# Kernel optimization log

Measured on AMD Instinct MI355X. Metric: run time of the kernel, lower is better.

Reference implementation:

```python
import jax, jax.numpy as jnp
import numpy as np

B = 2
SP = (480, 360, 32)   # spatial_shape (z, y, x)
GS = (8, 8, 8)        # query_gs_ratio
EP = (40, 15, 16)     # embed_params (pool compress ratio)
H = 8
N = 120000
D = 256
OUT = 20


def _dims(rat):
    return tuple((s + r - 1) // r for s, r in zip(SP, rat))


def sine_pe(coords, d_pos):
    # coords: [M,3] float voxel coords in original grid units; normalized sine PE
    nf = d_pos // 6
    sp = jnp.asarray(SP, jnp.float32)
    cn = coords / sp * (2.0 * jnp.pi)                      # normalize=True
    t = 10000.0 ** (jnp.arange(nf, dtype=jnp.float32) / nf)
    ang = cn[:, :, None] / t                               # [M,3,nf]
    pe = jnp.concatenate([jnp.sin(ang), jnp.cos(ang)], -1).reshape(coords.shape[0], -1)
    return jnp.pad(pe, ((0, 0), (0, d_pos - 6 * nf)))


def setup_inputs() -> dict:
    key = jax.random.key(0)
    ks = jax.random.split(key, 24)
    idx_b = jax.random.randint(ks[0], (N, 1), 0, B)
    idx_z = jax.random.randint(ks[1], (N, 1), 0, SP[0])
    idx_y = jax.random.randint(ks[2], (N, 1), 0, SP[1])
    idx_x = jax.random.randint(ks[3], (N, 1), 0, SP[2])
    indices = jnp.concatenate([idx_b, idx_z, idx_y, idx_x], axis=1).astype(jnp.int32)
    s = D ** -0.5
    p = lambda k, sh: jax.random.normal(k, sh, jnp.float32) * s
    return {
        'features': jax.random.normal(ks[4], (N, D), jnp.float32),
        'W_pool': p(ks[5], (D, D)), 'b_pool': jnp.zeros((D,), jnp.float32),
        'W_emb': p(ks[6], (D, D)), 'b_emb': jnp.zeros((D,), jnp.float32),
        'Wq': p(ks[7], (D, D)), 'bq': jnp.zeros((D,), jnp.float32),
        'Wk': p(ks[8], (D, D)), 'bk': jnp.zeros((D,), jnp.float32),
        'Wv': p(ks[9], (D, D)), 'bv': jnp.zeros((D,), jnp.float32),
        'Wo': p(ks[10], (D, D)), 'bo': jnp.zeros((D,), jnp.float32),
        'ln_g': jnp.ones((D,), jnp.float32), 'ln_b': jnp.zeros((D,), jnp.float32),
        'W_seg': p(ks[11], (D, OUT)), 'b_seg': jnp.zeros((OUT,), jnp.float32),
        'indices': indices,
        'batch_size': B,
    }


def reference(features, W_pool, b_pool, W_emb, b_emb, Wq, bq, Wk, bk, Wv, bv,
              Wo, bo, ln_g, ln_b, W_seg, b_seg, indices, batch_size):
    Zd, Yd, Xd = _dims(GS)
    Gq = Zd * Yd * Xd
    Sq = batch_size * Gq
    Ze, Ye, Xe = _dims(EP)
    Gk = Ze * Ye * Xe
    Sk = batch_size * Gk
    n = features.shape[0]

    # --- query pool branch: linear -> voxel-grid scatter_max ---
    pf = features @ W_pool + b_pool                                    # [N,D]
    dq = indices[:, 1:] // jnp.asarray(GS, jnp.int32)
    seg_q = ((indices[:, 0] * Zd + dq[:, 0]) * Yd + dq[:, 1]) * Xd + dq[:, 2]
    pool_max = jax.ops.segment_max(pf, seg_q, num_segments=Sq)
    cnt_q = jax.ops.segment_sum(jnp.ones((n,), jnp.float32), seg_q, num_segments=Sq)
    mq = cnt_q > 0
    pool_max = jnp.where(mq[:, None], pool_max, 0.0)
    cell = jnp.arange(Sq)
    rem = cell % Gq
    pool_c = jnp.stack([(rem // (Yd * Xd)) * GS[0],
                        ((rem // Xd) % Yd) * GS[1],
                        (rem % Xd) * GS[2]], -1).astype(jnp.float32)   # [Sq,3]

    # --- embedding branch ('pool'): linear -> coarse scatter_max + per-channel argmax coords ---
    ef = features @ W_emb + b_emb                                      # [N,D]
    de = indices[:, 1:] // jnp.asarray(EP, jnp.int32)
    seg_k = ((indices[:, 0] * Ze + de[:, 0]) * Ye + de[:, 1]) * Xe + de[:, 2]
    emb_max = jax.ops.segment_max(ef, seg_k, num_segments=Sk)
    cnt_k = jax.ops.segment_sum(jnp.ones((n,), jnp.float32), seg_k, num_segments=Sk)
    mk = cnt_k > 0
    emb_max = jnp.where(mk[:, None], emb_max, 0.0)
    winner = ef == jnp.where(mk[:, None], emb_max, -jnp.inf)[seg_k]
    idx = jax.ops.segment_max(jnp.where(winner, jnp.arange(n)[:, None], -1), seg_k, num_segments=Sk)
    idx_c = jnp.clip(idx, 0, n - 1)                                    # [Sk,D]
    ec = de.astype(jnp.float32)                                        # [N,3] downsampled coords
    emb_c = ec[idx_c].mean(axis=1) * jnp.asarray(EP, jnp.float32)      # [Sk,3]

    # --- position encoding (pointwise sine PE; per-batch loop in torch is pointwise-equivalent) ---
    pool_max = pool_max + sine_pe(pool_c, D)
    emb_max = emb_max + sine_pe(emb_c, D)

    # --- multi-head cross-attention (Q=pool, K/V=embedding), per-batch via dense grid reshape ---
    q_in = pool_max.reshape(batch_size, Gq, D)
    kv_in = emb_max.reshape(batch_size, Gk, D)
    dh = D // H
    q = (q_in @ Wq + bq).reshape(batch_size, Gq, H, dh)
    k = (kv_in @ Wk + bk).reshape(batch_size, Gk, H, dh)
    v = (kv_in @ Wv + bv).reshape(batch_size, Gk, H, dh)
    scores = jnp.einsum('bqhd,bkhd->bhqk', q, k) / jnp.float32(dh) ** 0.5
    kmask = mk.reshape(batch_size, Gk)
    scores = jnp.where(kmask[:, None, None, :], scores, -1e9)
    attn = jax.nn.softmax(scores, axis=-1)
    o = jnp.einsum('bhqk,bkhd->bqhd', attn, v).reshape(batch_size, Gq, D) @ Wo + bo
    h = q_in + o                                                       # residual + LayerNorm sublayer
    mu = h.mean(-1, keepdims=True)
    var = h.var(-1, keepdims=True)
    h = (h - mu) * jax.lax.rsqrt(var + 1e-5) * ln_g + ln_b
    feats_mhca = h.reshape(Sq, D)

    # --- gather back to voxels via pool_inv, residual, seg head (center-tap of SubMConv3d) ---
    vox = features + feats_mhca[seg_q]
    logits = vox @ W_seg + b_seg
    return logits
```

## Files before the change

kernel.cpp:

```cpp
#include <hip/hip_runtime.h>
#include <math.h>

#define N_PTS 120000
#define D 256
#define BATCH 2
#define NH 8
#define DH 32
#define OUTC 20

#define Zd 60
#define Yd 45
#define Xd 4
#define Gq 10800
#define Sq 21600

#define Ze 12
#define Ye 24
#define Xe 2
#define Gk 576
#define Sk 1152

typedef __bf16 bf16_t;
typedef __attribute__((ext_vector_type(8))) __bf16 bf16x8;
typedef __attribute__((ext_vector_type(4))) __bf16 bf16x4;
typedef __attribute__((ext_vector_type(4))) float f32x4;

__global__ __launch_bounds__(256) void k_prep(
    const float* __restrict__ Wp, const float* __restrict__ We,
    const float* __restrict__ Wq, const float* __restrict__ Wk,
    const float* __restrict__ Wv, const float* __restrict__ Wo,
    const float* __restrict__ bp, const float* __restrict__ be,
    const float* __restrict__ bk, const float* __restrict__ bv,
    const float* __restrict__ Wseg, const float* __restrict__ bseg,
    bf16_t* __restrict__ Wpe, bf16_t* __restrict__ Wqt,
    bf16_t* __restrict__ Wkv, bf16_t* __restrict__ Wot,
    bf16_t* __restrict__ Wsegt,
    float* __restrict__ bpe, float* __restrict__ bkv,
    float* __restrict__ bsegp)
{
    int n = blockIdx.x, k = threadIdx.x;
    if (n < 512) {
        const float* S = (n < 256) ? Wp : We;
        int nn = n & 255;
        Wpe[n * 256 + k] = (bf16_t)S[k * 256 + nn];
    } else if (n < 768) {
        int nn = n - 512;
        Wqt[nn * 256 + k] = (bf16_t)Wq[k * 256 + nn];
    } else if (n < 1280) {
        int m2 = n - 768;
        const float* S = (m2 < 256) ? Wk : Wv;
        int nn = m2 & 255;
        Wkv[m2 * 256 + k] = (bf16_t)S[k * 256 + nn];
    } else if (n < 1536) {
        int nn = n - 1280;
        Wot[nn * 256 + k] = (bf16_t)Wo[k * 256 + nn];
    } else if (n == 1536) {
        bpe[k] = bp[k]; bpe[256 + k] = be[k];
        bkv[k] = bk[k]; bkv[256 + k] = bv[k];
        if (k < 32) bsegp[k] = (k < OUTC) ? bseg[k] : 0.f;
    } else {
        int n2 = n - 1537;
        Wsegt[n2 * 256 + k] = (n2 < OUTC) ? (bf16_t)Wseg[k * OUTC + n2] : (bf16_t)0.f;
    }
}

__global__ __launch_bounds__(256) void k_count(
    const int* __restrict__ indices, int* __restrict__ cnt_q, int* __restrict__ cnt_k,
    int* __restrict__ segq, int* __restrict__ segk)
{
    int i = blockIdx.x * 256 + threadIdx.x;
    if (i >= N_PTS) return;
    const int* id = indices + (size_t)i * 4;
    int b = id[0], z = id[1], y = id[2], x = id[3];
    int sq = ((b * Zd + (z >> 3)) * Yd + (y >> 3)) * Xd + (x >> 3);
    int sk = ((b * Ze + (z / 40)) * Ye + (y / 15)) * Xe + (x >> 4);
    segq[i] = sq; segk[i] = sk;
    atomicAdd(&cnt_q[sq], 1);
    atomicAdd(&cnt_k[sk], 1);
}

__global__ __launch_bounds__(1024) void k_scan(
    const int* __restrict__ cnt, int n, int* __restrict__ offs, int* __restrict__ cursor)
{
    __shared__ int wbase[17];
    __shared__ int carry_s;
    const int t = threadIdx.x, lane = t & 63, w = t >> 6;
    if (t == 0) carry_s = 0;
    __syncthreads();
    for (int base = 0; base < n; base += 1024) {
        int v = (base + t < n) ? cnt[base + t] : 0;
        int incl = v;
        #pragma unroll
        for (int off = 1; off < 64; off <<= 1) {
            int u = __shfl_up(incl, off);
            if (lane >= off) incl += u;
        }
        if (lane == 63) wbase[w + 1] = incl;
        __syncthreads();
        if (t == 0) {
            int s = 0;
            wbase[0] = 0;
            #pragma unroll
            for (int i = 1; i <= 16; ++i) { s += wbase[i]; wbase[i] = s; }
        }
        __syncthreads();
        int excl = incl - v + wbase[w] + carry_s;
        if (base + t < n) { offs[base + t] = excl; cursor[base + t] = excl; }
        __syncthreads();
        if (t == 0) carry_s += wbase[16];
        __syncthreads();
    }
}

__global__ __launch_bounds__(256) void k_place(
    const int* __restrict__ segq, const int* __restrict__ segk,
    int* __restrict__ cur_q, int* __restrict__ cur_k,
    int* __restrict__ ids_q, int* __restrict__ ids_k)
{
    int i = blockIdx.x * 256 + threadIdx.x;
    if (i >= N_PTS) return;
    ids_q[atomicAdd(&cur_q[segq[i]], 1)] = i;
    ids_k[atomicAdd(&cur_k[segk[i]], 1)] = i;
}

__global__ __launch_bounds__(512, 2) void k_gemm(
    const float* __restrict__ A, int M,
    const bf16_t* __restrict__ Wt, const float* __restrict__ bias,
    int mode, float* __restrict__ outp, int ldo)
{
    __shared__ __align__(16) bf16_t Abuf[128][72];
    __shared__ __align__(16) bf16_t Bbuf[256][72];

    const int t = threadIdx.x;
    const int wave = t >> 6, lane = t & 63;
    const int wr = wave >> 2, wc = wave & 3;
    const int lrow = lane & 15, quad = lane >> 4;
    const int row0 = blockIdx.y * 128;
    const int ntile = blockIdx.x;

    f32x4 acc[4][4];
    #pragma unroll
    for (int mi = 0; mi < 4; ++mi)
        #pragma unroll
        for (int ni = 0; ni < 4; ++ni)
            acc[mi][ni] = (f32x4){0.f, 0.f, 0.f, 0.f};

    for (int k0 = 0; k0 < 256; k0 += 64) {
        #pragma unroll
        for (int i = 0; i < 4; ++i) {
            int c = i * 512 + t;
            int r = c >> 4, c4 = c & 15;
            float4 v = make_float4(0.f, 0.f, 0.f, 0.f);
            if (row0 + r < M)
                v = *(const float4*)(A + (size_t)(row0 + r) * 256 + k0 + c4 * 4);
            bf16x4 bv4;
            bv4[0] = (bf16_t)v.x; bv4[1] = (bf16_t)v.y;
            bv4[2] = (bf16_t)v.z; bv4[3] = (bf16_t)v.w;
            *(bf16x4*)&Abuf[r][c4 * 4] = bv4;
        }
        #pragma unroll
        for (int i = 0; i < 4; ++i) {
            int c = i * 512 + t;
            int r = c >> 3, c8 = c & 7;
            uint4 w = *(const uint4*)(Wt + ((size_t)(ntile * 256 + r)) * 256 + k0 + c8 * 8);
            *(uint4*)&Bbuf[r][c8 * 8] = w;
        }
        __syncthreads();

        #pragma unroll
        for (int kk = 0; kk < 64; kk += 32) {
            bf16x8 Af[4], Bf[4];
            #pragma unroll
            for (int mi = 0; mi < 4; ++mi)
                Af[mi] = *(const bf16x8*)&Abuf[wr * 64 + mi * 16 + lrow][kk + quad * 8];
            #pragma unroll
            for (int ni = 0; ni < 4; ++ni)
                Bf[ni] = *(const bf16x8*)&Bbuf[wc * 64 + ni * 16 + lrow][kk + quad * 8];
            #pragma unroll
            for (int mi = 0; mi < 4; ++mi)
                #pragma unroll
                for (int ni = 0; ni < 4; ++ni)
                    acc[mi][ni] = __builtin_amdgcn_mfma_f32_16x16x32_bf16(
                        Af[mi], Bf[ni], acc[mi][ni], 0, 0, 0);
        }
        __syncthreads();
    }

    const int colb = ntile * 256 + wc * 64;
    float biasv[4];
    #pragma unroll
    for (int ni = 0; ni < 4; ++ni) biasv[ni] = bias[colb + ni * 16 + lrow];

    if (mode == 0) {
        #pragma unroll
        for (int mi = 0; mi < 4; ++mi) {
            int lr = wr * 64 + mi * 16 + quad * 4;
            #pragma unroll
            for (int reg = 0; reg < 4; ++reg) {
                int grow = row0 + lr + reg;
                if (grow >= M) continue;
                #pragma unroll
                for (int ni = 0; ni < 4; ++ni) {
                    int col = colb + ni * 16 + lrow;
                    outp[(size_t)grow * ldo + col] = acc[mi][ni][reg] + biasv[ni];
                }
            }
        }
    } else {
        bf16_t* outb = (bf16_t*)outp;
        #pragma unroll
        for (int mi = 0; mi < 4; ++mi) {
            int lr = wr * 64 + mi * 16 + quad * 4;
            #pragma unroll
            for (int reg = 0; reg < 4; ++reg) {
                int grow = row0 + lr + reg;
                if (grow >= M) continue;
                #pragma unroll
                for (int ni = 0; ni < 4; ++ni) {
                    int col = colb + ni * 16 + lrow;
                    outb[(size_t)grow * ldo + col] = (bf16_t)(acc[mi][ni][reg] + biasv[ni]);
                }
            }
        }
    }
}

__device__ inline float pe_val(int j, float cz, float cy, float cx) {
    if (j >= 252) return 0.f;
    int dim = j / 84;
    int f = j % 84;
    int fi = (f >= 42) ? (f - 42) : f;
    float c  = (dim == 0) ? cz : ((dim == 1) ? cy : cx);
    float sp = (dim == 0) ? 480.f : ((dim == 1) ? 360.f : 32.f);
    float cn = c / sp * 6.28318530717958647692f;
    float tt = expf((float)fi * (9.210340371976184f / 42.f));
    float ang = cn / tt;
    return (f >= 42) ? cosf(ang) : sinf(ang);
}

__global__ __launch_bounds__(256) void k_pool_q(
    const bf16_t* __restrict__ pfb, const int* __restrict__ ids,
    const int* __restrict__ offs, const int* __restrict__ cnt,
    float* __restrict__ out)
{
    const int t = threadIdx.x, lane = t & 63, w = t >> 6;
    const int s = blockIdx.x * 4 + w;
    if (s >= Sq) return;
    const int count = cnt[s], start = offs[s];
    float mx[4] = {-3.0e38f, -3.0e38f, -3.0e38f, -3.0e38f};
    for (int r = 0; r < count; ++r) {
        int i = ids[start + r];
        bf16x4 v = *(const bf16x4*)(pfb + (size_t)i * 256 + lane * 4);
        #pragma unroll
        for (int j = 0; j < 4; ++j) mx[j] = fmaxf(mx[j], (float)v[j]);
    }
    int rem = s % Gq;
    float cz = (float)((rem / (Yd * Xd)) * 8);
    float cy = (float)(((rem / Xd) % Yd) * 8);
    float cx = (float)((rem % Xd) * 8);
    #pragma unroll
    for (int j = 0; j < 4; ++j) {
        float v = (count > 0) ? mx[j] : 0.f;
        out[(size_t)s * 256 + lane * 4 + j] = v + pe_val(lane * 4 + j, cz, cy, cx);
    }
}

__global__ __launch_bounds__(512) void k_pool_k(
    const bf16_t* __restrict__ efb, const int* __restrict__ ids,
    const int* __restrict__ offs, const int* __restrict__ cnt,
    float* __restrict__ out, int* __restrict__ kmask)
{
    __shared__ float red[8][256];
    const int t = threadIdx.x, lane = t & 63, w = t >> 6;
    const int s = blockIdx.x;
    const int count = cnt[s], start = offs[s];
    float mx[4] = {-3.0e38f, -3.0e38f, -3.0e38f, -3.0e38f};
    for (int r = w; r < count; r += 8) {
        int i = ids[start + r];
        bf16x4 v = *(const bf16x4*)(efb + (size_t)i * 256 + lane * 4);
        #pragma unroll
        for (int j = 0; j < 4; ++j) mx[j] = fmaxf(mx[j], (float)v[j]);
    }
    #pragma unroll
    for (int j = 0; j < 4; ++j) red[w][lane * 4 + j] = mx[j];
    __syncthreads();
    if (t < 256) {
        float m = red[0][t];
        #pragma unroll
        for (int i = 1; i < 8; ++i) m = fmaxf(m, red[i][t]);
        if (count == 0) m = 0.f;
        int rem = s % Gk;
        float cz = (float)((rem / (Ye * Xe)) * 40);
        float cy = (float)(((rem / Xe) % Ye) * 15);
        float cx = (float)((rem % Xe) * 16);
        out[(size_t)s * 256 + t] = m + pe_val(t, cz, cy, cx);
        if (t == 0) kmask[s] = (count > 0) ? 1 : 0;
    }
}

__global__ __launch_bounds__(256) void k_attn_mfma(
    const bf16_t* __restrict__ Q, const bf16_t* __restrict__ KV,
    const int* __restrict__ kmask, float* __restrict__ O)
{
    __shared__ __align__(16) bf16_t Qs[64][40];
    __shared__ __align__(16) bf16_t Ks[192][40];
    __shared__ __align__(16) bf16_t Vts[32][200];
    __shared__ __align__(16) bf16_t Ps[4][16][200];
    __shared__ float mskf[192];

    const int bh = blockIdx.y;
    const int b = bh >> 3, h = bh & 7;
    const int t = threadIdx.x, wave = t >> 6, lane = t & 63;
    const int lrow = lane & 15, quad = lane >> 4;
    const int q0 = blockIdx.x * 64;

    {
        int r = t >> 2, part = t & 3;
        int qi = q0 + r;
        uint4 val = make_uint4(0u, 0u, 0u, 0u);
        if (qi < Gq)
            val = *(const uint4*)(Q + ((size_t)(b * Gq + qi)) * 256 + h * 32 + part * 8);
        *(uint4*)&Qs[r][part * 8] = val;
    }
    __syncthreads();

    const bf16x8 Aq = *(const bf16x8*)&Qs[wave * 16 + lrow][quad * 8];

    f32x4 oacc[2];
    oacc[0] = (f32x4){0.f, 0.f, 0.f, 0.f};
    oacc[1] = (f32x4){0.f, 0.f, 0.f, 0.f};
    float m_run[4], l_run[4];
    #pragma unroll
    for (int r = 0; r < 4; ++r) { m_run[r] = -3.0e38f; l_run[r] = 0.f; }

    for (int c0 = 0; c0 < Gk; c0 += 192) {
        __syncthreads();
        #pragma unroll
        for (int i = 0; i < 3; ++i) {
            int idx = i * 256 + t;
            int kk = idx >> 2, part = idx & 3;
            uint4 val = *(const uint4*)(KV + ((size_t)(b * Gk + c0 + kk)) * 512 + h * 32 + part * 8);
            *(uint4*)&Ks[kk][part * 8] = val;
        }
        #pragma unroll
        for (int i = 0; i < 3; ++i) {
            int idx = i * 256 + t;
            int kk = idx >> 2, part = idx & 3;
            bf16x8 v = *(const bf16x8*)(KV + ((size_t)(b * Gk + c0 + kk)) * 512 + 256 + h * 32 + part * 8);
            #pragma unroll
            for (int j = 0; j < 8; ++j)
                Vts[part * 8 + j][kk] = v[j];
        }
        if (t < 192) mskf[t] = kmask[b * Gk + c0 + t] ? 0.f : -1.0e9f;
        __syncthreads();

        float sreg[12][4];
        #pragma unroll
        for (int nt = 0; nt < 12; ++nt) {
            bf16x8 Bk = *(const bf16x8*)&Ks[nt * 16 + lrow][quad * 8];
            f32x4 sacc = __builtin_amdgcn_mfma_f32_16x16x32_bf16(
                Aq, Bk, (f32x4){0.f, 0.f, 0.f, 0.f}, 0, 0, 0);
            float pen = mskf[nt * 16 + lrow];
            #pragma unroll
            for (int r = 0; r < 4; ++r)
                sreg[nt][r] = sacc[r] * 0.17677669529663688f + pen;
        }

        float alpha[4];
        #pragma unroll
        for (int r = 0; r < 4; ++r) {
            float mx = sreg[0][r];
            #pragma unroll
            for (int nt = 1; nt < 12; ++nt) mx = fmaxf(mx, sreg[nt][r]);
            #pragma unroll
            for (int off = 1; off < 16; off <<= 1)
                mx = fmaxf(mx, __shfl_xor(mx, off));
            float mnew = fmaxf(m_run[r], mx);
            alpha[r] = __expf(m_run[r] - mnew);
            m_run[r] = mnew;
            l_run[r] *= alpha[r];
        }
        #pragma unroll
        for (int n2 = 0; n2 < 2; ++n2)
            #pragma unroll
            for (int r = 0; r < 4; ++r) oacc[n2][r] *= alpha[r];

        float psum[4] = {0.f, 0.f, 0.f, 0.f};
        #pragma unroll
        for (int nt = 0; nt < 12; ++nt) {
            #pragma unroll
            for (int r = 0; r < 4; ++r) {
                float p = __expf(sreg[nt][r] - m_run[r]);
                psum[r] += p;
                Ps[wave][quad * 4 + r][nt * 16 + lrow] = (bf16_t)p;
            }
        }
        #pragma unroll
        for (int r = 0; r < 4; ++r) {
            float s = psum[r];
            #pragma unroll
            for (int off = 1; off < 16; off <<= 1) s += __shfl_xor(s, off);
            l_run[r] += s;
        }

        #pragma unroll
        for (int ks = 0; ks < 6; ++ks) {
            bf16x8 Ap = *(const bf16x8*)&Ps[wave][lrow][ks * 32 + quad * 8];
            #pragma unroll
            for (int n2 = 0; n2 < 2; ++n2) {
                bf16x8 Bv = *(const bf16x8*)&Vts[n2 * 16 + lrow][ks * 32 + quad * 8];
                oacc[n2] = __builtin_amdgcn_mfma_f32_16x16x32_bf16(
                    Ap, Bv, oacc[n2], 0, 0, 0);
            }
        }
    }

    #pragma unroll
    for (int r = 0; r < 4; ++r) {
        int qi = q0 + wave * 16 + quad * 4 + r;
        if (qi >= Gq) continue;
        float inv = (l_run[r] > 0.f) ? (1.f / l_run[r]) : 0.f;
        #pragma unroll
        for (int n2 = 0; n2 < 2; ++n2)
            O[((size_t)(b * Gq + qi)) * 256 + h * 32 + n2 * 16 + lrow] = oacc[n2][r] * inv;
    }
}

__global__ __launch_bounds__(256) void k_ln(
    const float* __restrict__ oproj, const float* __restrict__ resid,
    const float* __restrict__ g, const float* __restrict__ bta,
    float* __restrict__ out)
{
    const int s = blockIdx.x, t = threadIdx.x;
    float h = resid[(size_t)s * D + t] + oproj[(size_t)s * D + t];

    float s1 = h, s2 = h * h;
    for (int o = 32; o > 0; o >>= 1) {
        s1 += __shfl_down(s1, o);
        s2 += __shfl_down(s2, o);
    }
    __shared__ float r1[4], r2[4];
    __shared__ float mu_s, rstd_s;
    int w = t >> 6;
    if ((t & 63) == 0) { r1[w] = s1; r2[w] = s2; }
    __syncthreads();
    if (t == 0) {
        float a = r1[0] + r1[1] + r1[2] + r1[3];
        float bsum = r2[0] + r2[1] + r2[2] + r2[3];
        float mu = a * (1.f / 256.f);
        float var = bsum * (1.f / 256.f) - mu * mu;
        mu_s = mu;
        rstd_s = rsqrtf(var + 1e-5f);
    }
    __syncthreads();
    out[(size_t)s * D + t] = (h - mu_s) * rstd_s * g[t] + bta[t];
}

__global__ __launch_bounds__(512, 2) void k_logits_mfma(
    const float* __restrict__ feat, const float* __restrict__ mhca,
    const int* __restrict__ indices, const bf16_t* __restrict__ Wsegt,
    const float* __restrict__ bsegp, float* __restrict__ out)
{
    __shared__ __align__(16) bf16_t Abuf[128][72];
    __shared__ __align__(16) bf16_t Bbuf[32][72];
    __shared__ int sq_s[128];

    const int t = threadIdx.x;
    const int wave = t >> 6, lane = t & 63;
    const int lrow = lane & 15, quad = lane >> 4;
    const int row0 = blockIdx.x * 128;

    if (t < 128) {
        int row = row0 + t;
        if (row < N_PTS) {
            const int* id = indices + (size_t)row * 4;
            sq_s[t] = ((id[0] * Zd + (id[1] >> 3)) * Yd + (id[2] >> 3)) * Xd + (id[3] >> 3);
        } else sq_s[t] = 0;
    }
    __syncthreads();

    f32x4 acc[2];
    acc[0] = (f32x4){0.f, 0.f, 0.f, 0.f};
    acc[1] = (f32x4){0.f, 0.f, 0.f, 0.f};

    for (int k0 = 0; k0 < 256; k0 += 64) {
        #pragma unroll
        for (int i = 0; i < 4; ++i) {
            int c = i * 512 + t;
            int r = c >> 4, c4 = c & 15;
            float4 v = make_float4(0.f, 0.f, 0.f, 0.f);
            int grow = row0 + r;
            if (grow < N_PTS) {
                v = *(const float4*)(feat + (size_t)grow * 256 + k0 + c4 * 4);
                float4 m = *(const float4*)(mhca + (size_t)sq_s[r] * 256 + k0 + c4 * 4);
                v.x += m.x; v.y += m.y; v.z += m.z; v.w += m.w;
            }
            bf16x4 bv4;
            bv4[0] = (bf16_t)v.x; bv4[1] = (bf16_t)v.y;
            bv4[2] = (bf16_t)v.z; bv4[3] = (bf16_t)v.w;
            *(bf16x4*)&Abuf[r][c4 * 4] = bv4;
        }
        if (t < 256) {
            int r = t >> 3, c8 = t & 7;
            uint4 w = *(const uint4*)(Wsegt + (size_t)r * 256 + k0 + c8 * 8);
            *(uint4*)&Bbuf[r][c8 * 8] = w;
        }
        __syncthreads();

        #pragma unroll
        for (int kk = 0; kk < 64; kk += 32) {
            bf16x8 Af = *(const bf16x8*)&Abuf[wave * 16 + lrow][kk + quad * 8];
            #pragma unroll
            for (int ni = 0; ni < 2; ++ni) {
                bf16x8 Bf = *(const bf16x8*)&Bbuf[ni * 16 + lrow][kk + quad * 8];
                acc[ni] = __builtin_amdgcn_mfma_f32_16x16x32_bf16(
                    Af, Bf, acc[ni], 0, 0, 0);
            }
        }
        __syncthreads();
    }

    #pragma unroll
    for (int ni = 0; ni < 2; ++ni) {
        int col = ni * 16 + lrow;
        if (col >= OUTC) continue;
        float bias = bsegp[col];
        #pragma unroll
        for (int reg = 0; reg < 4; ++reg) {
            int grow = row0 + wave * 16 + quad * 4 + reg;
            if (grow >= N_PTS) continue;
            out[(size_t)grow * OUTC + col] = acc[ni][reg] + bias;
        }
    }
}

extern "C" void kernel_launch(void* const* d_in, const int* in_sizes, int n_in,
                              void* d_out, int out_size, void* d_ws, size_t ws_size,
                              hipStream_t stream) {
    const float* features = (const float*)d_in[0];
    const float* W_pool = (const float*)d_in[1];
    const float* b_pool = (const float*)d_in[2];
    const float* W_emb  = (const float*)d_in[3];
    const float* b_emb  = (const float*)d_in[4];
    const float* Wq = (const float*)d_in[5];
    const float* bq = (const float*)d_in[6];
    const float* Wk = (const float*)d_in[7];
    const float* bk = (const float*)d_in[8];
    const float* Wv = (const float*)d_in[9];
    const float* bv = (const float*)d_in[10];
    const float* Wo = (const float*)d_in[11];
    const float* bo = (const float*)d_in[12];
    const float* ln_g = (const float*)d_in[13];
    const float* ln_b = (const float*)d_in[14];
    const float* W_seg = (const float*)d_in[15];
    const float* b_seg = (const float*)d_in[16];
    const int* indices = (const int*)d_in[17];
    float* out = (float*)d_out;

    float* ws = (float*)d_ws;
    const size_t SQD = (size_t)Sq * D;
    const size_t SKD = (size_t)Sk * D;
    const size_t PFB_FL = (size_t)N_PTS * D / 2;

    size_t oP   = 0;
    size_t oPF  = oP + PFB_FL;
    size_t oEF  = oPF + SQD;
    size_t oWpe = oEF + SKD;
    size_t oWqt = oWpe + 65536;
    size_t oWkv = oWqt + 32768;
    size_t oWot = oWkv + 65536;
    size_t obpe = oWot + 32768;
    size_t obkv = obpe + 512;
    size_t oCnt = obkv + 512;
    size_t oOffq = oCnt + 21600 + 1152;
    size_t oCurq = oOffq + 21600;
    size_t oOffk = oCurq + 21600;
    size_t oCurk = oOffk + 1152;
    size_t oSegq = oCurk + 1152;
    size_t oSegk = oSegq + N_PTS;
    size_t oIdsq = oSegk + N_PTS;
    size_t oIdsk = oIdsq + N_PTS;
    size_t oKm   = oIdsk + N_PTS;
    size_t oWst  = oKm + 1152;
    size_t obsg  = oWst + 4096;

    bf16_t* pfb = (bf16_t*)(ws + oP);
    float* pool_feat = ws + oPF;
    float* emb_feat  = ws + oEF;
    bf16_t* Wpe = (bf16_t*)(ws + oWpe);
    bf16_t* Wqt = (bf16_t*)(ws + oWqt);
    bf16_t* Wkv = (bf16_t*)(ws + oWkv);
    bf16_t* Wot = (bf16_t*)(ws + oWot);
    float* bpe = ws + obpe;
    float* bkv = ws + obkv;
    int* cnt_q = (int*)(ws + oCnt);
    int* cnt_k = cnt_q + 21600;
    int* offs_q = (int*)(ws + oOffq);
    int* cur_q  = (int*)(ws + oCurq);
    int* offs_k = (int*)(ws + oOffk);
    int* cur_k  = (int*)(ws + oCurk);
    int* segq = (int*)(ws + oSegq);
    int* segk = (int*)(ws + oSegk);
    int* ids_q = (int*)(ws + oIdsq);
    int* ids_k = (int*)(ws + oIdsk);
    int* kmask = (int*)(ws + oKm);
    bf16_t* Wsegt = (bf16_t*)(ws + oWst);
    float* bsegp = ws + obsg;

    bf16_t* Qb  = (bf16_t*)(ws + oP);
    bf16_t* KVb = (bf16_t*)(ws + oP + 2764800);
    float* attnO = ws + oP + 3059712;
    float* oproj = ws + oP + 8589312;
    float* mhca  = ws + oP + 3059712;

    hipMemsetAsync(cnt_q, 0, (21600 + 1152) * sizeof(int), stream);

    k_prep<<<1569, 256, 0, stream>>>(W_pool, W_emb, Wq, Wk, Wv, Wo,
                                     b_pool, b_emb, bk, bv, W_seg, b_seg,
                                     Wpe, Wqt, Wkv, Wot, Wsegt, bpe, bkv, bsegp);

    k_count<<<(N_PTS + 255) / 256, 256, 0, stream>>>(indices, cnt_q, cnt_k, segq, segk);
    k_scan<<<1, 1024, 0, stream>>>(cnt_q, 21600, offs_q, cur_q);
    k_scan<<<1, 1024, 0, stream>>>(cnt_k, 1152, offs_k, cur_k);
    k_place<<<(N_PTS + 255) / 256, 256, 0, stream>>>(segq, segk, cur_q, cur_k, ids_q, ids_k);

    {
        dim3 g(1, (N_PTS + 127) / 128);
        k_gemm<<<g, 512, 0, stream>>>(features, N_PTS, Wpe + 256 * 256, bpe + 256, 2,
                                      (float*)pfb, 256);
    }
    k_pool_k<<<Sk, 512, 0, stream>>>(pfb, ids_k, offs_k, cnt_k, emb_feat, kmask);

    {
        dim3 g(1, (N_PTS + 127) / 128);
        k_gemm<<<g, 512, 0, stream>>>(features, N_PTS, Wpe, bpe, 2,
                                      (float*)pfb, 256);
    }
    k_pool_q<<<(Sq + 3) / 4, 256, 0, stream>>>(pfb, ids_q, offs_q, cnt_q, pool_feat);

    {
        dim3 g(1, (Sq + 127) / 128);
        k_gemm<<<g, 512, 0, stream>>>(pool_feat, Sq, Wqt, bq, 2, (float*)Qb, 256);
    }
    {
        dim3 g(2, (Sk + 127) / 128);
        k_gemm<<<g, 512, 0, stream>>>(emb_feat, Sk, Wkv, bkv, 2, (float*)KVb, 512);
    }

    {
        dim3 ag((Gq + 63) / 64, BATCH * NH);
        k_attn_mfma<<<ag, 256, 0, stream>>>(Qb, KVb, kmask, attnO);
    }

    {
        dim3 g(1, (Sq + 127) / 128);
        k_gemm<<<g, 512, 0, stream>>>(attnO, Sq, Wot, bo, 0, oproj, 256);
    }

    k_ln<<<Sq, 256, 0, stream>>>(oproj, pool_feat, ln_g, ln_b, mhca);

    k_logits_mfma<<<(N_PTS + 127) / 128, 512, 0, stream>>>(
        features, mhca, indices, Wsegt, bsegp, out);
}
```

Baseline: 603.4 us.

## Pre-cast features to bf16 and use direct-to-LDS bf16 GEMM for voxel projections

Adds a kernel that casts the 120k×256 fp32 feature matrix to bf16 once. The two large per-voxel projection GEMMs then read the bf16 copy through a new GEMM kernel that uses global_load_lds to fill shared memory directly, with a 128×128 tile and a 2-wide column grid. The aim is to halve the A-operand traffic across the two GEMMs and skip per-element conversion in the inner loop. The cost is an extra cast pass and extra workspace, and the fast path is taken only when the workspace is large enough; the GEMM loop has no double-buffering.

Result: no change. 594.2 us (-1.5%).

```diff
diff --git a/kernel.cpp b/kernel.cpp
--- a/kernel.cpp
+++ b/kernel.cpp
@@ -24,6 +24,13 @@
 typedef __attribute__((ext_vector_type(8))) __bf16 bf16x8;
 typedef __attribute__((ext_vector_type(4))) __bf16 bf16x4;
 typedef __attribute__((ext_vector_type(4))) float f32x4;
+
+__device__ __forceinline__ void glds16(const void* g, void* l) {
+    __builtin_amdgcn_global_load_lds(
+        (const __attribute__((address_space(1))) unsigned int*)g,
+        (__attribute__((address_space(3))) unsigned int*)l,
+        16, 0, 0);
+}
 
 __global__ __launch_bounds__(256) void k_prep(
     const float* __restrict__ Wp, const float* __restrict__ We,
@@ -64,6 +71,21 @@
     }
 }
 
+__global__ __launch_bounds__(256) void k_cast(
+    const float* __restrict__ in, bf16_t* __restrict__ out)
+{
+    const size_t total = (size_t)N_PTS * 32;
+    const size_t stride = (size_t)gridDim.x * 256;
+    for (size_t i = (size_t)blockIdx.x * 256 + threadIdx.x; i < total; i += stride) {
+        float4 a = *(const float4*)(in + i * 8);
+        float4 b = *(const float4*)(in + i * 8 + 4);
+        bf16x8 o;
+        o[0] = (bf16_t)a.x; o[1] = (bf16_t)a.y; o[2] = (bf16_t)a.z; o[3] = (bf16_t)a.w;
+        o[4] = (bf16_t)b.x; o[5] = (bf16_t)b.y; o[6] = (bf16_t)b.z; o[7] = (bf16_t)b.w;
+        *(bf16x8*)(out + i * 8) = o;
+    }
+}
+
 __global__ __launch_bounds__(256) void k_count(
     const int* __restrict__ indices, int* __restrict__ cnt_q, int* __restrict__ cnt_k,
     int* __restrict__ segq, int* __restrict__ segk)
@@ -121,6 +143,87 @@
     if (i >= N_PTS) return;
     ids_q[atomicAdd(&cur_q[segq[i]], 1)] = i;
     ids_k[atomicAdd(&cur_k[segk[i]], 1)] = i;
+}
+
+__global__ __launch_bounds__(256) void k_gemm_bf(
+    const bf16_t* __restrict__ A, int M,
+    const bf16_t* __restrict__ Wt, const float* __restrict__ bias,
+    bf16_t* __restrict__ outb, int ldo)
+{
+    __shared__ __align__(16) bf16_t Abuf[128 * 64];
+    __shared__ __align__(16) bf16_t Bbuf[128 * 64];
+
+    const int t = threadIdx.x;
+    const int wave = t >> 6, lane = t & 63;
+    const int wr = wave >> 1, wc = wave & 1;
+    const int lrow = lane & 15, quad = lane >> 4;
+    const int lr8 = lane >> 3, lc8 = lane & 7;
+    const int row0 = blockIdx.y * 128;
+    const int ntile = blockIdx.x;
+
+    f32x4 acc[4][4];
+    #pragma unroll
+    for (int mi = 0; mi < 4; ++mi)
+        #pragma unroll
+        for (int ni = 0; ni < 4; ++ni)
+            acc[mi][ni] = (f32x4){0.f, 0.f, 0.f, 0.f};
+
+    for (int k0 = 0; k0 < 256; k0 += 64) {
+        #pragma unroll
+        for (int i = 0; i < 4; ++i) {
+            int chunk = wave * 4 + i;
+            int rowA = row0 + chunk * 8 + lr8;
+            if (rowA > M - 1) rowA = M - 1;
+            glds16(A + (size_t)rowA * 256 + k0 + lc8 * 8, &Abuf[chunk * 512]);
+        }
+        #pragma unroll
+        for (int i = 0; i < 4; ++i) {
+            int chunk = wave * 4 + i;
+            glds16(Wt + (size_t)(ntile * 128 + chunk * 8 + lr8) * 256 + k0 + lc8 * 8,
+                   &Bbuf[chunk * 512]);
+        }
+        asm volatile("s_waitcnt vmcnt(0)" ::: "memory");
+        __builtin_amdgcn_sched_barrier(0);
+        __syncthreads();
+
+        #pragma unroll
+        for (int kk = 0; kk < 64; kk += 32) {
+            bf16x8 Af[4], Bf[4];
+            #pragma unroll
+            for (int mi = 0; mi < 4; ++mi)
+                Af[mi] = *(const bf16x8*)&Abuf[(wr * 64 + mi * 16 + lrow) * 64 + kk + quad * 8];
+            #pragma unroll
+            for (int ni = 0; ni < 4; ++ni)
+                Bf[ni] = *(const bf16x8*)&Bbuf[(wc * 64 + ni * 16 + lrow) * 64 + kk + quad * 8];
+            #pragma unroll
+            for (int mi = 0; mi < 4; ++mi)
+                #pragma unroll
+                for (int ni = 0; ni < 4; ++ni)
+                    acc[mi][ni] = __builtin_amdgcn_mfma_f32_16x16x32_bf16(
+                        Af[mi], Bf[ni], acc[mi][ni], 0, 0, 0);
+        }
+        __syncthreads();
+    }
+
+    const int colb = ntile * 128 + wc * 64;
+    float biasv[4];
+    #pragma unroll
+    for (int ni = 0; ni < 4; ++ni) biasv[ni] = bias[colb + ni * 16 + lrow];
+
+    #pragma unroll
+    for (int mi = 0; mi < 4; ++mi) {
+        int lr = wr * 64 + mi * 16 + quad * 4;
+        #pragma unroll
+        for (int reg = 0; reg < 4; ++reg) {
+            int grow = row0 + lr + reg;
+            if (grow >= M) continue;
+            #pragma unroll
+            for (int ni = 0; ni < 4; ++ni) {
+                int col = colb + ni * 16 + lrow;
+                outb[(size_t)grow * ldo + col] = (bf16_t)(acc[mi][ni][reg] + biasv[ni]);
+            }
+        }
+    }
 }
 
 __global__ __launch_bounds__(512, 2) void k_gemm(
@@ -583,6 +686,7 @@
     size_t oKm   = oIdsk + N_PTS;
     size_t oWst  = oKm + 1152;
     size_t obsg  = oWst + 4096;
+    size_t oFB   = obsg + 32;
 
     bf16_t* pfb = (bf16_t*)(ws + oP);
     float* pool_feat = ws + oPF;
@@ -606,6 +710,7 @@
     int* kmask = (int*)(ws + oKm);
     bf16_t* Wsegt = (bf16_t*)(ws + oWst);
     float* bsegp = ws + obsg;
+    bf16_t* fb16 = (bf16_t*)(ws + oFB);
 
     bf16_t* Qb  = (bf16_t*)(ws + oP);
     bf16_t* KVb = (bf16_t*)(ws + oP + 2764800);
@@ -613,25 +718,37 @@
     float* oproj = ws + oP + 8589312;
     float* mhca  = ws + oP + 3059712;
 
+    const bool fast = ws_size >= (oFB + PFB_FL) * sizeof(float);
+
     hipMemsetAsync(cnt_q, 0, (21600 + 1152) * sizeof(int), stream);
 
     k_prep<<<1569, 256, 0, stream>>>(W_pool, W_emb, Wq, Wk, Wv, Wo,
                                      b_pool, b_emb, bk, bv, W_seg, b_seg,
                                      Wpe, Wqt, Wkv, Wot, Wsegt, bpe, bkv, bsegp);
+
+    if (fast)
+        k_cast<<<2048, 256, 0, stream>>>(features, fb16);
 
     k_count<<<(N_PTS + 255) / 256, 256, 0, stream>>>(indices, cnt_q, cnt_k, segq, segk);
     k_scan<<<1, 1024, 0, stream>>>(cnt_q, 21600, offs_q, cur_q);
     k_scan<<<1, 1024, 0, stream>>>(cnt_k, 1152, offs_k, cur_k);
     k_place<<<(N_PTS + 255) / 256, 256, 0, stream>>>(segq, segk, cur_q, cur_k, ids_q, ids_k);
 
-    {
+    if (fast) {
+        dim3 g(2, (N_PTS + 127) / 128);
+        k_gemm_bf<<<g, 256, 0, stream>>>(fb16, N_PTS, Wpe + 256 * 256, bpe + 256,
+                                         pfb, 256);
+    } else {
         dim3 g(1, (N_PTS + 127) / 128);
         k_gemm<<<g, 512, 0, stream>>>(features, N_PTS, Wpe + 256 * 256, bpe + 256, 2,
                                       (float*)pfb, 256);
     }
     k_pool_k<<<Sk, 512, 0, stream>>>(pfb, ids_k, offs_k, cnt_k, emb_feat, kmask);
 
-    {
+    if (fast) {
+        dim3 g(2, (N_PTS + 127) / 128);
+        k_gemm_bf<<<g, 256, 0, stream>>>(fb16, N_PTS, Wpe, bpe, pfb, 256);
+    } else {
         dim3 g(1, (N_PTS + 127) / 128);
         k_gemm<<<g, 512, 0, stream>>>(features, N_PTS, Wpe, bpe, 2,
                                       (float*)pfb, 256);
```
